# Kernel tuning notes

Hardware: AMD Instinct MI355X
Metric: run time of the kernel (lower is better)

The kernel has to match this reference:

```python
import jax, jax.numpy as jnp
import numpy as np


def setup_inputs() -> dict:
    key = jax.random.key(0)
    k1, k2 = jax.random.split(key)
    B, Q, T, D = 128, 512, 512, 256
    inputs = jax.random.normal(k1, (B, T, D), dtype=jnp.float32)
    query = jax.random.normal(k2, (B, Q, D), dtype=jnp.float32)
    return {"inputs": inputs, "query": query}


def reference(inputs, query):
    # inputs: [B, T, D] (keys == values), query: [B, Q, D]
    D = inputs.shape[2]
    scale = 1.0 / jnp.sqrt(jnp.asarray(D, dtype=inputs.dtype))
    # scores: [B, Q, T]
    scores = jnp.einsum("bqd,btd->bqt", query, inputs) * scale
    weights = jax.nn.softmax(scores, axis=2)
    # attended: [B, Q, D]
    attended = jnp.einsum("bqt,btd->bqd", weights, inputs)
    # pool over query dim -> [B, D]
    return jnp.sum(attended, axis=1)
```

## Files before the change

### kernel.cpp

```cpp
#include <hip/hip_runtime.h>
#include <hip/hip_bf16.h>


typedef __bf16 bf16x8 __attribute__((ext_vector_type(8)));
typedef float  f32x4  __attribute__((ext_vector_type(4)));

#define B_    128
#define Tn    512
#define Dn    256
#define SCALE 0.0625f
#define IMG_BYTES ((size_t)B_ * 8 * 32768)

__device__ __forceinline__ int gpos(int row, int ch) {
  return row * 32 + ((ch ^ row) & 31);
}

__device__ __forceinline__ void async_copy16(void* lds, const void* g) {
  __builtin_amdgcn_global_load_lds(
      (const __attribute__((address_space(1))) unsigned int*)g,
      (__attribute__((address_space(3))) unsigned int*)lds, 16, 0, 0);
}

__global__ void __launch_bounds__(256) prep(const float* __restrict__ inputs,
                                            __bf16* __restrict__ img) {
  const int bid = blockIdx.x;
  const int b = bid & 127, tt = bid >> 7;
  const int tid = threadIdx.x;
  const float* src = inputs + ((size_t)b * Tn + (size_t)tt * 64) * Dn;
  __bf16* dst = img + ((size_t)(b * 8 + tt)) * 16384;
#pragma unroll
  for (int i = 0; i < 8; ++i) {
    int g = i * 256 + tid;
    int row = g >> 5, pos = g & 31;
    int ch = (pos ^ row) & 31;
    const float4* p = (const float4*)(src + row * 256 + ch * 8);
    float4 v0 = p[0], v1 = p[1];
    bf16x8 w;
    w[0] = (__bf16)v0.x; w[1] = (__bf16)v0.y;
    w[2] = (__bf16)v0.z; w[3] = (__bf16)v0.w;
    w[4] = (__bf16)v1.x; w[5] = (__bf16)v1.y;
    w[6] = (__bf16)v1.z; w[7] = (__bf16)v1.w;
    *(bf16x8*)(dst + (size_t)g * 8) = w;
  }
}

__global__ void __launch_bounds__(512, 2) attn_qk(
    const __bf16* __restrict__ img, const float* __restrict__ query,
    float* __restrict__ c_ws) {
  __shared__ __bf16 Kb[2][64 * 256];

  const int tid  = threadIdx.x;
  const int bidx = blockIdx.x;
  const int b  = bidx & 127;
  const int qt = bidx >> 7;

  const float*  qsrc = query + ((size_t)b * 512 + (size_t)qt * 128) * Dn;
  const __bf16* kimg = img + (size_t)b * 8 * 16384;

  const int wave = tid >> 6, lane = tid & 63;
  const int quad = lane >> 4, l15 = lane & 15;

#pragma unroll
  for (int i = 0; i < 4; ++i) {
    int off = (wave * 4 + i) * 512 + lane * 8;
    async_copy16((void*)((__bf16*)Kb[0] + off), (const void*)(kimg + off));
  }

  bf16x8 afrag[8];
#pragma unroll
  for (int dc = 0; dc < 8; ++dc) {
    const float4* p =
        (const float4*)(qsrc + (wave * 16 + l15) * 256 + dc * 32 + quad * 8);
    float4 v0 = p[0], v1 = p[1];
    bf16x8 w;
    w[0] = (__bf16)v0.x; w[1] = (__bf16)v0.y;
    w[2] = (__bf16)v0.z; w[3] = (__bf16)v0.w;
    w[4] = (__bf16)v1.x; w[5] = (__bf16)v1.y;
    w[6] = (__bf16)v1.z; w[7] = (__bf16)v1.w;
    afrag[dc] = w;
  }
  __syncthreads();

  f32x4 acc[8][4];
  f32x4 zero = {0.f, 0.f, 0.f, 0.f};
#pragma unroll
  for (int tt = 0; tt < 8; ++tt)
#pragma unroll
    for (int ct = 0; ct < 4; ++ct) acc[tt][ct] = zero;

#pragma unroll
  for (int tt = 0; tt < 8; ++tt) {
    if (tt < 7) {
      const __bf16* nsrc = kimg + (size_t)(tt + 1) * 16384;
      __bf16* ndst = (__bf16*)Kb[(tt + 1) & 1];
#pragma unroll
      for (int i = 0; i < 4; ++i) {
        int off = (wave * 4 + i) * 512 + lane * 8;
        async_copy16((void*)(ndst + off), (const void*)(nsrc + off));
      }
    }
    const __bf16* cur = Kb[tt & 1];
#pragma unroll
    for (int dc = 0; dc < 8; ++dc) {
#pragma unroll
      for (int ct = 0; ct < 4; ++ct) {
        bf16x8 bb =
            *(const bf16x8*)(cur + gpos(ct * 16 + l15, dc * 4 + quad) * 8);
        acc[tt][ct] = __builtin_amdgcn_mfma_f32_16x16x32_bf16(
            afrag[dc], bb, acc[tt][ct], 0, 0, 0);
      }
    }
    __syncthreads();
  }

  float rs[4] = {0.f, 0.f, 0.f, 0.f};
#pragma unroll
  for (int tt = 0; tt < 8; ++tt)
#pragma unroll
    for (int ct = 0; ct < 4; ++ct)
#pragma unroll
      for (int r = 0; r < 4; ++r) {
        float p = __expf(acc[tt][ct][r] * SCALE);
        acc[tt][ct][r] = p;
        rs[r] += p;
      }
#pragma unroll
  for (int off = 1; off <= 8; off <<= 1)
#pragma unroll
    for (int r = 0; r < 4; ++r) rs[r] += __shfl_xor(rs[r], off);
  float linv[4];
#pragma unroll
  for (int r = 0; r < 4; ++r) linv[r] = 1.f / rs[r];

  float* cpart = (float*)Kb;
#pragma unroll
  for (int tt = 0; tt < 8; ++tt)
#pragma unroll
    for (int ct = 0; ct < 4; ++ct) {
      float v = acc[tt][ct][0] * linv[0] + acc[tt][ct][1] * linv[1] +
                acc[tt][ct][2] * linv[2] + acc[tt][ct][3] * linv[3];
      v += __shfl_xor(v, 16);
      v += __shfl_xor(v, 32);
      if (quad == 0) cpart[wave * 512 + tt * 64 + ct * 16 + l15] = v;
    }
  __syncthreads();

  float csum = 0.f;
#pragma unroll
  for (int w = 0; w < 8; ++w) csum += cpart[w * 512 + tid];
  c_ws[((size_t)qt * B_ + b) * Tn + tid] = csum;
}

__global__ void __launch_bounds__(256) attn_av(
    const __bf16* __restrict__ img, const float* __restrict__ c_ws,
    float* __restrict__ out) {
  __shared__ float cs[256];
  __shared__ float psum[4][256];
  const int bid = blockIdx.x;
  const int b = bid & 127, th = bid >> 7;
  const int tid = threadIdx.x;
  const int wave = tid >> 6, lane = tid & 63;
  const int ch = lane & 31, phase = lane >> 5;

  {
    int t = th * 256 + tid;
    cs[tid] = c_ws[(size_t)(0 * B_ + b) * Tn + t] +
              c_ws[(size_t)(1 * B_ + b) * Tn + t] +
              c_ws[(size_t)(2 * B_ + b) * Tn + t] +
              c_ws[(size_t)(3 * B_ + b) * Tn + t];
  }
  __syncthreads();

  const __bf16* tile = img + (size_t)(b * 8 + th * 4 + wave) * 16384;
  float o[8] = {0.f, 0.f, 0.f, 0.f, 0.f, 0.f, 0.f, 0.f};
#pragma unroll
  for (int j = 0; j < 32; ++j) {
    int row = j * 2 + phase;
    float c = cs[wave * 64 + row];
    bf16x8 v = *(const bf16x8*)(tile + gpos(row, ch) * 8);
#pragma unroll
    for (int k = 0; k < 8; ++k) o[k] += c * (float)v[k];
  }
#pragma unroll
  for (int k = 0; k < 8; ++k) o[k] += __shfl_xor(o[k], 32);
  if (phase == 0) {
#pragma unroll
    for (int k = 0; k < 8; ++k) psum[wave][ch * 8 + k] = o[k];
  }
  __syncthreads();

  float s = psum[0][tid] + psum[1][tid] + psum[2][tid] + psum[3][tid];
  atomicAdd(out + b * 256 + tid, s);
}

extern "C" void kernel_launch(void* const* d_in, const int* in_sizes, int n_in,
                              void* d_out, int out_size, void* d_ws, size_t ws_size,
                              hipStream_t stream) {
  const float* inputs = (const float*)d_in[0];
  const float* query  = (const float*)d_in[1];
  float* out = (float*)d_out;
  __bf16* img = (__bf16*)d_ws;
  float* c_ws = (float*)((char*)d_ws + IMG_BYTES);

  hipMemsetAsync(out, 0, (size_t)B_ * Dn * sizeof(float), stream);
  prep<<<dim3(1024), dim3(256), 0, stream>>>(inputs, img);
  attn_qk<<<dim3(512), dim3(512), 0, stream>>>(img, query, c_ws);
  attn_av<<<dim3(256), dim3(256), 0, stream>>>(img, c_ws, out);
}
```

Before: 190.4 us.

## Fuse prep, QK and AV kernels into one with last-block reduction

Removes the separate bf16 conversion pass and AV kernel. K tiles are now read as fp32 straight from inputs into registers, converted and stored to swizzled LDS while the MFMA loop runs, replacing the async global-to-LDS copies. The last of the four query-tile blocks per batch, found with an atomic counter, computes the weighted sum over V in fp32 and writes the output directly, so the memset of out and the output atomics go away. The cost is register-staged prefetch with more VGPR pressure (launch_bounds min-blocks hint dropped), an fp32 K read in every block, and a serial tail done by only 128 blocks.

Result: slower. 252.1 us (+32.4%).

```diff
diff --git a/kernel.cpp b/kernel.cpp
--- a/kernel.cpp
+++ b/kernel.cpp
@@ -9,62 +9,59 @@
 #define Tn    512
 #define Dn    256
 #define SCALE 0.0625f
-#define IMG_BYTES ((size_t)B_ * 8 * 32768)
 
-__device__ __forceinline__ int gpos(int row, int ch) {
-  return row * 32 + ((ch ^ row) & 31);
+__device__ __forceinline__ int lidx(int row, int ch) {
+  return row * 256 + (((ch ^ row) & 31) << 3);
 }
 
-__device__ __forceinline__ void async_copy16(void* lds, const void* g) {
-  __builtin_amdgcn_global_load_lds(
-      (const __attribute__((address_space(1))) unsigned int*)g,
-      (__attribute__((address_space(3))) unsigned int*)lds, 16, 0, 0);
+__device__ __forceinline__ void kload(const float* __restrict__ src, int tid,
+                                      float4* pre) {
+#pragma unroll
+  for (int i = 0; i < 4; ++i) {
+    int u = i * 512 + tid;
+    int row = u >> 5, ch = u & 31;
+    const float4* p = (const float4*)(src + row * 256 + ch * 8);
+    pre[2 * i]     = p[0];
+    pre[2 * i + 1] = p[1];
+  }
 }
 
-__global__ void __launch_bounds__(256) prep(const float* __restrict__ inputs,
-                                            __bf16* __restrict__ img) {
-  const int bid = blockIdx.x;
-  const int b = bid & 127, tt = bid >> 7;
-  const int tid = threadIdx.x;
-  const float* src = inputs + ((size_t)b * Tn + (size_t)tt * 64) * Dn;
-  __bf16* dst = img + ((size_t)(b * 8 + tt)) * 16384;
+__device__ __forceinline__ void kstore(__bf16* dst, int tid,
+                                       const float4* pre) {
 #pragma unroll
-  for (int i = 0; i < 8; ++i) {
-    int g = i * 256 + tid;
-    int row = g >> 5, pos = g & 31;
-    int ch = (pos ^ row) & 31;
-    const float4* p = (const float4*)(src + row * 256 + ch * 8);
-    float4 v0 = p[0], v1 = p[1];
+  for (int i = 0; i < 4; ++i) {
+    int u = i * 512 + tid;
+    int row = u >> 5, ch = u & 31;
+    float4 v0 = pre[2 * i], v1 = pre[2 * i + 1];
     bf16x8 w;
     w[0] = (__bf16)v0.x; w[1] = (__bf16)v0.y;
     w[2] = (__bf16)v0.z; w[3] = (__bf16)v0.w;
     w[4] = (__bf16)v1.x; w[5] = (__bf16)v1.y;
     w[6] = (__bf16)v1.z; w[7] = (__bf16)v1.w;
-    *(bf16x8*)(dst + (size_t)g * 8) = w;
+    *(bf16x8*)(dst + lidx(row, ch)) = w;
   }
 }
 
-__global__ void __launch_bounds__(512, 2) attn_qk(
-    const __bf16* __restrict__ img, const float* __restrict__ query,
-    float* __restrict__ c_ws) {
+__global__ void __launch_bounds__(512) attn_fused(
+    const float* __restrict__ inputs, const float* __restrict__ query,
+    float* __restrict__ out, float* __restrict__ c_ws,
+    unsigned int* __restrict__ done) {
   __shared__ __bf16 Kb[2][64 * 256];
+  __shared__ unsigned int prev_s;
 
   const int tid  = threadIdx.x;
   const int bidx = blockIdx.x;
   const int b  = bidx & 127;
   const int qt = bidx >> 7;
 
-  const float*  qsrc = query + ((size_t)b * 512 + (size_t)qt * 128) * Dn;
-  const __bf16* kimg = img + (size_t)b * 8 * 16384;
+  const float* qsrc = query  + ((size_t)b * 512 + (size_t)qt * 128) * Dn;
+  const float* ksrc = inputs + (size_t)b * Tn * Dn;
 
   const int wave = tid >> 6, lane = tid & 63;
   const int quad = lane >> 4, l15 = lane & 15;
 
-#pragma unroll
-  for (int i = 0; i < 4; ++i) {
-    int off = (wave * 4 + i) * 512 + lane * 8;
-    async_copy16((void*)((__bf16*)Kb[0] + off), (const void*)(kimg + off));
-  }
+  float4 pre[8];
+  kload(ksrc, tid, pre);
 
   bf16x8 afrag[8];
 #pragma unroll
@@ -79,6 +76,8 @@
     w[6] = (__bf16)v1.z; w[7] = (__bf16)v1.w;
     afrag[dc] = w;
   }
+
+  kstore((__bf16*)Kb[0], tid, pre);
   __syncthreads();
 
   f32x4 acc[8][4];
@@ -90,26 +89,19 @@
 
 #pragma unroll
   for (int tt = 0; tt < 8; ++tt) {
-    if (tt < 7) {
-      const __bf16* nsrc = kimg + (size_t)(tt + 1) * 16384;
-      __bf16* ndst = (__bf16*)Kb[(tt + 1) & 1];
-#pragma unroll
-      for (int i = 0; i < 4; ++i) {
-        int off = (wave * 4 + i) * 512 + lane * 8;
-        async_copy16((void*)(ndst + off), (const void*)(nsrc + off));
-      }
-    }
+    if (tt < 7) kload(ksrc + (size_t)(tt + 1) * 64 * Dn, tid, pre);
     const __bf16* cur = Kb[tt & 1];
 #pragma unroll
     for (int dc = 0; dc < 8; ++dc) {
 #pragma unroll
       for (int ct = 0; ct < 4; ++ct) {
         bf16x8 bb =
-            *(const bf16x8*)(cur + gpos(ct * 16 + l15, dc * 4 + quad) * 8);
+            *(const bf16x8*)(cur + lidx(ct * 16 + l15, dc * 4 + quad));
         acc[tt][ct] = __builtin_amdgcn_mfma_f32_16x16x32_bf16(
             afrag[dc], bb, acc[tt][ct], 0, 0, 0);
       }
     }
+    if (tt < 7) kstore((__bf16*)Kb[(tt + 1) & 1], tid, pre);
     __syncthreads();
   }
 
@@ -132,7 +124,7 @@
 #pragma unroll
   for (int r = 0; r < 4; ++r) linv[r] = 1.f / rs[r];
 
-  float* cpart = (float*)Kb;
+  float* cpart = (float*)Kb[0];
 #pragma unroll
   for (int tt = 0; tt < 8; ++tt)
 #pragma unroll
@@ -145,52 +137,48 @@
     }
   __syncthreads();
 
-  float csum = 0.f;
+  {
+    float csum = 0.f;
 #pragma unroll
-  for (int w = 0; w < 8; ++w) csum += cpart[w * 512 + tid];
-  c_ws[((size_t)qt * B_ + b) * Tn + tid] = csum;
-}
+    for (int w = 0; w < 8; ++w) csum += cpart[w * 512 + tid];
+    c_ws[((size_t)qt * B_ + b) * Tn + tid] = csum;
+  }
 
-__global__ void __launch_bounds__(256) attn_av(
-    const __bf16* __restrict__ img, const float* __restrict__ c_ws,
-    float* __restrict__ out) {
-  __shared__ float cs[256];
-  __shared__ float psum[4][256];
-  const int bid = blockIdx.x;
-  const int b = bid & 127, th = bid >> 7;
-  const int tid = threadIdx.x;
-  const int wave = tid >> 6, lane = tid & 63;
-  const int ch = lane & 31, phase = lane >> 5;
+  __threadfence();
+  __syncthreads();
+  if (tid == 0) prev_s = atomicAdd(&done[b], 1u);
+  __syncthreads();
+  if (prev_s != 3u) return;
+  __threadfence();
 
+  float* cs   = (float*)Kb[1];
+  float* psum = (float*)Kb[1] + 512;
+  cs[tid] = c_ws[(size_t)(0 * B_ + b) * Tn + tid] +
+            c_ws[(size_t)(1 * B_ + b) * Tn + tid] +
+            c_ws[(size_t)(2 * B_ + b) * Tn + tid] +
+            c_ws[(size_t)(3 * B_ + b) * Tn + tid];
+  __syncthreads();
+
+  const float4* vb =
+      (const float4*)(inputs + ((size_t)b * Tn + wave * 64) * Dn) + lane;
+  float ox = 0.f, oy = 0.f, oz = 0.f, ow = 0.f;
+#pragma unroll 8
+  for (int j = 0; j < 64; ++j) {
+    float c = cs[wave * 64 + j];
+    float4 v = vb[(size_t)j * 64];
+    ox += c * v.x; oy += c * v.y; oz += c * v.z; ow += c * v.w;
+  }
   {
-    int t = th * 256 + tid;
-    cs[tid] = c_ws[(size_t)(0 * B_ + b) * Tn + t] +
-              c_ws[(size_t)(1 * B_ + b) * Tn + t] +
-              c_ws[(size_t)(2 * B_ + b) * Tn + t] +
-              c_ws[(size_t)(3 * B_ + b) * Tn + t];
+    float4 t = {ox, oy, oz, ow};
+    *(float4*)&psum[wave * 256 + lane * 4] = t;
   }
   __syncthreads();
-
-  const __bf16* tile = img + (size_t)(b * 8 + th * 4 + wave) * 16384;
-  float o[8] = {0.f, 0.f, 0.f, 0.f, 0.f, 0.f, 0.f, 0.f};
+  if (tid < 256) {
+    float s = 0.f;
 #pragma unroll
-  for (int j = 0; j < 32; ++j) {
-    int row = j * 2 + phase;
-    float c = cs[wave * 64 + row];
-    bf16x8 v = *(const bf16x8*)(tile + gpos(row, ch) * 8);
-#pragma unroll
-    for (int k = 0; k < 8; ++k) o[k] += c * (float)v[k];
+    for (int w = 0; w < 8; ++w) s += psum[w * 256 + tid];
+    out[b * 256 + tid] = s;
   }
-#pragma unroll
-  for (int k = 0; k < 8; ++k) o[k] += __shfl_xor(o[k], 32);
-  if (phase == 0) {
-#pragma unroll
-    for (int k = 0; k < 8; ++k) psum[wave][ch * 8 + k] = o[k];
-  }
-  __syncthreads();
-
-  float s = psum[0][tid] + psum[1][tid] + psum[2][tid] + psum[3][tid];
-  atomicAdd(out + b * 256 + tid, s);
 }
 
 extern "C" void kernel_launch(void* const* d_in, const int* in_sizes, int n_in,
@@ -198,12 +186,12 @@
                               hipStream_t stream) {
   const float* inputs = (const float*)d_in[0];
   const float* query  = (const float*)d_in[1];
-  float* out = (float*)d_out;
-  __bf16* img = (__bf16*)d_ws;
-  float* c_ws = (float*)((char*)d_ws + IMG_BYTES);
+  float* out  = (float*)d_out;
+  float* c_ws = (float*)d_ws;
+  unsigned int* done =
+      (unsigned int*)((char*)d_ws + (size_t)4 * B_ * Tn * sizeof(float));
 
-  hipMemsetAsync(out, 0, (size_t)B_ * Dn * sizeof(float), stream);
-  prep<<<dim3(1024), dim3(256), 0, stream>>>(inputs, img);
-  attn_qk<<<dim3(512), dim3(512), 0, stream>>>(img, query, c_ws);
-  attn_av<<<dim3(256), dim3(256), 0, stream>>>(img, c_ws, out);
+  hipMemsetAsync(done, 0, B_ * sizeof(unsigned int), stream);
+  attn_fused<<<dim3(512), dim3(512), 0, stream>>>(inputs, query, out, c_ws,
+                                                  done);
 }
```

## Pre-swizzle K into MFMA fragment order and load directly to registers

Applied to the files above, without the earlier changes.

The prep kernel now writes the bf16 key image in MFMA B-fragment order, so attn_qk reads fragments straight from global memory into double-buffered registers instead of staging through LDS with async copies and barriers. This removes LDS traffic and per-tile syncs but raises register pressure (32 accumulators plus 16 fragment vectors) and drops the occupancy hint. attn_av now reads the original fp32 inputs with 1024 blocks over 64-row slices, which adds parallelism but doubles the bytes read per element and quadruples the atomics.

New measurement: 255.0 us. 1.34x slower.

```diff
diff --git a/kernel.cpp b/kernel.cpp
--- a/kernel.cpp
+++ b/kernel.cpp
@@ -9,17 +9,7 @@
 #define Tn    512
 #define Dn    256
 #define SCALE 0.0625f
-#define IMG_BYTES ((size_t)B_ * 8 * 32768)
-
-__device__ __forceinline__ int gpos(int row, int ch) {
-  return row * 32 + ((ch ^ row) & 31);
-}
-
-__device__ __forceinline__ void async_copy16(void* lds, const void* g) {
-  __builtin_amdgcn_global_load_lds(
-      (const __attribute__((address_space(1))) unsigned int*)g,
-      (__attribute__((address_space(3))) unsigned int*)lds, 16, 0, 0);
-}
+#define IMG_ELEMS ((size_t)Tn * Dn)
 
 __global__ void __launch_bounds__(256) prep(const float* __restrict__ inputs,
                                             __bf16* __restrict__ img) {
@@ -27,103 +17,90 @@
   const int b = bid & 127, tt = bid >> 7;
   const int tid = threadIdx.x;
   const float* src = inputs + ((size_t)b * Tn + (size_t)tt * 64) * Dn;
-  __bf16* dst = img + ((size_t)(b * 8 + tt)) * 16384;
+  __bf16* dst = img + (size_t)b * IMG_ELEMS + (size_t)tt * 16384;
 #pragma unroll
   for (int i = 0; i < 8; ++i) {
-    int g = i * 256 + tid;
-    int row = g >> 5, pos = g & 31;
-    int ch = (pos ^ row) & 31;
-    const float4* p = (const float4*)(src + row * 256 + ch * 8);
+    int u = i * 256 + tid;
+    int tgl = u >> 9;
+    int kc  = (u >> 6) & 7;
+    int l   = u & 63;
+    int t   = tgl * 16 + (l & 15);
+    int d   = kc * 32 + (l >> 4) * 8;
+    const float4* p = (const float4*)(src + t * 256 + d);
     float4 v0 = p[0], v1 = p[1];
     bf16x8 w;
     w[0] = (__bf16)v0.x; w[1] = (__bf16)v0.y;
     w[2] = (__bf16)v0.z; w[3] = (__bf16)v0.w;
     w[4] = (__bf16)v1.x; w[5] = (__bf16)v1.y;
     w[6] = (__bf16)v1.z; w[7] = (__bf16)v1.w;
-    *(bf16x8*)(dst + (size_t)g * 8) = w;
+    *(bf16x8*)(dst + (size_t)u * 8) = w;
   }
 }
 
-__global__ void __launch_bounds__(512, 2) attn_qk(
+__global__ void __launch_bounds__(512) attn_qk(
     const __bf16* __restrict__ img, const float* __restrict__ query,
     float* __restrict__ c_ws) {
-  __shared__ __bf16 Kb[2][64 * 256];
+  __shared__ float cpart[8 * 512];
 
   const int tid  = threadIdx.x;
   const int bidx = blockIdx.x;
   const int b  = bidx & 127;
   const int qt = bidx >> 7;
 
-  const float*  qsrc = query + ((size_t)b * 512 + (size_t)qt * 128) * Dn;
-  const __bf16* kimg = img + (size_t)b * 8 * 16384;
-
   const int wave = tid >> 6, lane = tid & 63;
   const int quad = lane >> 4, l15 = lane & 15;
 
-#pragma unroll
-  for (int i = 0; i < 4; ++i) {
-    int off = (wave * 4 + i) * 512 + lane * 8;
-    async_copy16((void*)((__bf16*)Kb[0] + off), (const void*)(kimg + off));
-  }
-
+  const float* qsrc = query + ((size_t)b * 512 + (size_t)qt * 128) * Dn;
   bf16x8 afrag[8];
 #pragma unroll
-  for (int dc = 0; dc < 8; ++dc) {
+  for (int kc = 0; kc < 8; ++kc) {
     const float4* p =
-        (const float4*)(qsrc + (wave * 16 + l15) * 256 + dc * 32 + quad * 8);
+        (const float4*)(qsrc + (wave * 16 + l15) * 256 + kc * 32 + quad * 8);
     float4 v0 = p[0], v1 = p[1];
     bf16x8 w;
     w[0] = (__bf16)v0.x; w[1] = (__bf16)v0.y;
     w[2] = (__bf16)v0.z; w[3] = (__bf16)v0.w;
     w[4] = (__bf16)v1.x; w[5] = (__bf16)v1.y;
     w[6] = (__bf16)v1.z; w[7] = (__bf16)v1.w;
-    afrag[dc] = w;
+    afrag[kc] = w;
   }
-  __syncthreads();
 
-  f32x4 acc[8][4];
+  const __bf16* kb = img + (size_t)b * IMG_ELEMS;
+
+  f32x4 acc[32];
   f32x4 zero = {0.f, 0.f, 0.f, 0.f};
 #pragma unroll
-  for (int tt = 0; tt < 8; ++tt)
+  for (int tg = 0; tg < 32; ++tg) acc[tg] = zero;
+
+  bf16x8 bfr[2][8];
 #pragma unroll
-    for (int ct = 0; ct < 4; ++ct) acc[tt][ct] = zero;
+  for (int kc = 0; kc < 8; ++kc)
+    bfr[0][kc] = *(const bf16x8*)(kb + ((size_t)(0 * 8 + kc) * 64 + lane) * 8);
 
 #pragma unroll
-  for (int tt = 0; tt < 8; ++tt) {
-    if (tt < 7) {
-      const __bf16* nsrc = kimg + (size_t)(tt + 1) * 16384;
-      __bf16* ndst = (__bf16*)Kb[(tt + 1) & 1];
+  for (int tg = 0; tg < 32; ++tg) {
+    const int cb = tg & 1, nb = cb ^ 1;
+    if (tg < 31) {
 #pragma unroll
-      for (int i = 0; i < 4; ++i) {
-        int off = (wave * 4 + i) * 512 + lane * 8;
-        async_copy16((void*)(ndst + off), (const void*)(nsrc + off));
-      }
+      for (int kc = 0; kc < 8; ++kc)
+        bfr[nb][kc] =
+            *(const bf16x8*)(kb + ((size_t)((tg + 1) * 8 + kc) * 64 + lane) * 8);
     }
-    const __bf16* cur = Kb[tt & 1];
 #pragma unroll
-    for (int dc = 0; dc < 8; ++dc) {
-#pragma unroll
-      for (int ct = 0; ct < 4; ++ct) {
-        bf16x8 bb =
-            *(const bf16x8*)(cur + gpos(ct * 16 + l15, dc * 4 + quad) * 8);
-        acc[tt][ct] = __builtin_amdgcn_mfma_f32_16x16x32_bf16(
-            afrag[dc], bb, acc[tt][ct], 0, 0, 0);
-      }
-    }
-    __syncthreads();
+    for (int kc = 0; kc < 8; ++kc)
+      acc[tg] = __builtin_amdgcn_mfma_f32_16x16x32_bf16(afrag[kc], bfr[cb][kc],
+                                                        acc[tg], 0, 0, 0);
   }
 
   float rs[4] = {0.f, 0.f, 0.f, 0.f};
 #pragma unroll
-  for (int tt = 0; tt < 8; ++tt)
+  for (int tg = 0; tg < 32; ++tg)
 #pragma unroll
-    for (int ct = 0; ct < 4; ++ct)
-#pragma unroll
-      for (int r = 0; r < 4; ++r) {
-        float p = __expf(acc[tt][ct][r] * SCALE);
-        acc[tt][ct][r] = p;
-        rs[r] += p;
-      }
+    for (int r = 0; r < 4; ++r) {
+      float p = __expf(acc[tg][r] * SCALE);
+      acc[tg][r] = p;
+      rs[r] += p;
+    }
 #pragma unroll
   for (int off = 1; off <= 8; off <<= 1)
 #pragma unroll
@@ -132,17 +109,14 @@
 #pragma unroll
   for (int r = 0; r < 4; ++r) linv[r] = 1.f / rs[r];
 
-  float* cpart = (float*)Kb;
 #pragma unroll
-  for (int tt = 0; tt < 8; ++tt)
-#pragma unroll
-    for (int ct = 0; ct < 4; ++ct) {
-      float v = acc[tt][ct][0] * linv[0] + acc[tt][ct][1] * linv[1] +
-                acc[tt][ct][2] * linv[2] + acc[tt][ct][3] * linv[3];
-      v += __shfl_xor(v, 16);
-      v += __shfl_xor(v, 32);
-      if (quad == 0) cpart[wave * 512 + tt * 64 + ct * 16 + l15] = v;
-    }
+  for (int tg = 0; tg < 32; ++tg) {
+    float v = acc[tg][0] * linv[0] + acc[tg][1] * linv[1] +
+              acc[tg][2] * linv[2] + acc[tg][3] * linv[3];
+    v += __shfl_xor(v, 16);
+    v += __shfl_xor(v, 32);
+    if (quad == 0) cpart[wave * 512 + tg * 16 + l15] = v;
+  }
   __syncthreads();
 
   float csum = 0.f;
@@ -152,18 +126,15 @@
 }
 
 __global__ void __launch_bounds__(256) attn_av(
-    const __bf16* __restrict__ img, const float* __restrict__ c_ws,
+    const float* __restrict__ inputs, const float* __restrict__ c_ws,
     float* __restrict__ out) {
-  __shared__ float cs[256];
-  __shared__ float psum[4][256];
-  const int bid = blockIdx.x;
-  const int b = bid & 127, th = bid >> 7;
-  const int tid = threadIdx.x;
-  const int wave = tid >> 6, lane = tid & 63;
-  const int ch = lane & 31, phase = lane >> 5;
+  __shared__ float cs[64];
+  __shared__ float psum[3][256];
+  const int bid = blockIdx.x, tid = threadIdx.x;
+  const int b = bid & 127, sl = bid >> 7;
 
-  {
-    int t = th * 256 + tid;
+  if (tid < 64) {
+    int t = sl * 64 + tid;
     cs[tid] = c_ws[(size_t)(0 * B_ + b) * Tn + t] +
               c_ws[(size_t)(1 * B_ + b) * Tn + t] +
               c_ws[(size_t)(2 * B_ + b) * Tn + t] +
@@ -171,26 +142,31 @@
   }
   __syncthreads();
 
-  const __bf16* tile = img + (size_t)(b * 8 + th * 4 + wave) * 16384;
-  float o[8] = {0.f, 0.f, 0.f, 0.f, 0.f, 0.f, 0.f, 0.f};
+  const int w = tid >> 6, d4 = tid & 63;
+  const float4* vb =
+      (const float4*)(inputs + ((size_t)b * Tn + sl * 64 + w * 16) * Dn) + d4;
+  float ox = 0.f, oy = 0.f, oz = 0.f, ow = 0.f;
 #pragma unroll
-  for (int j = 0; j < 32; ++j) {
-    int row = j * 2 + phase;
-    float c = cs[wave * 64 + row];
-    bf16x8 v = *(const bf16x8*)(tile + gpos(row, ch) * 8);
-#pragma unroll
-    for (int k = 0; k < 8; ++k) o[k] += c * (float)v[k];
+  for (int j = 0; j < 16; ++j) {
+    float c = cs[w * 16 + j];
+    float4 v = vb[(size_t)j * 64];
+    ox += c * v.x; oy += c * v.y; oz += c * v.z; ow += c * v.w;
   }
-#pragma unroll
-  for (int k = 0; k < 8; ++k) o[k] += __shfl_xor(o[k], 32);
-  if (phase == 0) {
-#pragma unroll
-    for (int k = 0; k < 8; ++k) psum[wave][ch * 8 + k] = o[k];
+  if (w) {
+    float4 t = {ox, oy, oz, ow};
+    *(float4*)&psum[w - 1][d4 * 4] = t;
   }
   __syncthreads();
-
-  float s = psum[0][tid] + psum[1][tid] + psum[2][tid] + psum[3][tid];
-  atomicAdd(out + b * 256 + tid, s);
+  if (!w) {
+    float4 p0 = *(float4*)&psum[0][d4 * 4];
+    float4 p1 = *(float4*)&psum[1][d4 * 4];
+    float4 p2 = *(float4*)&psum[2][d4 * 4];
+    float* op = out + b * 256 + d4 * 4;
+    atomicAdd(op + 0, ox + p0.x + p1.x + p2.x);
+    atomicAdd(op + 1, oy + p0.y + p1.y + p2.y);
+    atomicAdd(op + 2, oz + p0.z + p1.z + p2.z);
+    atomicAdd(op + 3, ow + p0.w + p1.w + p2.w);
+  }
 }
 
 extern "C" void kernel_launch(void* const* d_in, const int* in_sizes, int n_in,
@@ -200,10 +176,11 @@
   const float* query  = (const float*)d_in[1];
   float* out = (float*)d_out;
   __bf16* img = (__bf16*)d_ws;
-  float* c_ws = (float*)((char*)d_ws + IMG_BYTES);
+  float* c_ws =
+      (float*)((char*)d_ws + (size_t)B_ * IMG_ELEMS * sizeof(__bf16));
 
   hipMemsetAsync(out, 0, (size_t)B_ * Dn * sizeof(float), stream);
   prep<<<dim3(1024), dim3(256), 0, stream>>>(inputs, img);
   attn_qk<<<dim3(512), dim3(512), 0, stream>>>(img, query, c_ws);
-  attn_av<<<dim3(256), dim3(256), 0, stream>>>(img, c_ws, out);
+  attn_av<<<dim3(1024), dim3(256), 0, stream>>>(inputs, c_ws, out);
 }
```
